# Kernel optimization log

Measured on AMD Instinct MI355X. Metric: run time of the kernel, lower is better.

## Reference

```python
import jax, jax.numpy as jnp
import numpy as np

CONTEXT = 2048
D_MODEL = 1024
HEAD = 64


def setup_inputs() -> dict:
    key = jax.random.key(0)
    kx, kk, kq, kv = jax.random.split(key, 4)
    s = 1.0 / np.sqrt(D_MODEL)  # ~ torch Linear init scale
    return {
        "x": jax.random.normal(kx, (8, CONTEXT, D_MODEL), dtype=jnp.float32),
        "Wk": jax.random.uniform(kk, (D_MODEL, HEAD), dtype=jnp.float32, minval=-s, maxval=s),
        "Wq": jax.random.uniform(kq, (D_MODEL, HEAD), dtype=jnp.float32, minval=-s, maxval=s),
        "Wv": jax.random.uniform(kv, (D_MODEL, HEAD), dtype=jnp.float32, minval=-s, maxval=s),
    }


def reference(x, Wk, Wq, Wv):
    b, t, c = x.shape
    k = jnp.einsum("btc,ch->bth", x, Wk)
    q = jnp.einsum("btc,ch->bth", x, Wq)
    v = jnp.einsum("btc,ch->bth", x, Wv)
    # NOTE: original scales by c**-0.5 (embedding dim), not head_size**-0.5
    scores = jnp.einsum("bqh,bkh->bqk", q, k) * (c ** -0.5)
    causal = jnp.tril(jnp.ones((t, t), dtype=bool))
    scores = jnp.where(causal, scores, jnp.float32(-jnp.inf))
    weights = jax.nn.softmax(scores, axis=-1)
    return jnp.einsum("bqk,bkh->bqh", weights, v)
```

## Files before the change

kernel.cpp:

```cpp
#include <hip/hip_runtime.h>
#include <hip/hip_bf16.h>

#define CTX 2048
#define DM  1024
#define HD  64
#define BATCH 8
#define NSLOT 144

typedef __attribute__((ext_vector_type(8))) short bf16x8;
typedef __attribute__((ext_vector_type(4))) float f32x4;

__device__ inline unsigned short f2bf(float f) {
    unsigned int u = __float_as_uint(f);
    unsigned int r = (u + 0x7fffu + ((u >> 16) & 1u)) >> 16;
    return (unsigned short)r;
}

__device__ inline bf16x8 pack8(const float4& f0, const float4& f1) {
    union { bf16x8 v; __hip_bfloat162 h[4]; } u;
    u.h[0] = __float22bfloat162_rn(make_float2(f0.x, f0.y));
    u.h[1] = __float22bfloat162_rn(make_float2(f0.z, f0.w));
    u.h[2] = __float22bfloat162_rn(make_float2(f1.x, f1.y));
    u.h[3] = __float22bfloat162_rn(make_float2(f1.z, f1.w));
    return u.v;
}

__device__ __forceinline__ void gload16(const void* gsrc, void* ldst) {
    __builtin_amdgcn_global_load_lds(
        (const __attribute__((address_space(1))) void*)gsrc,
        (__attribute__((address_space(3))) void*)ldst,
        16, 0, 0);
}

__device__ __forceinline__ int chunk_prefix(int qi) {
    int q4 = qi >> 2, r = qi & 3;
    return qi + 2 * q4 * (q4 - 1) + q4 * r;
}

__global__ __launch_bounds__(256) void wtrans(
    const float* __restrict__ Wq, const float* __restrict__ Wk,
    const float* __restrict__ Wv, unsigned short* __restrict__ wt)
{
    __shared__ __align__(16) unsigned short tile[64][72];
    const int m  = blockIdx.y;
    const int k0 = blockIdx.x * 64;
    const float* W = (m == 0) ? Wq : (m == 1) ? Wk : Wv;
    const int tid = threadIdx.x;
    const int c   = tid & 63, kk = tid >> 6;
    #pragma unroll
    for (int i = 0; i < 16; i++) {
        int kl = kk + i * 4;
        tile[c][kl] = f2bf(W[(size_t)(k0 + kl) * HD + c]);
    }
    __syncthreads();
    const int c2 = tid >> 2, seg = tid & 3;
    bf16x8 a = *reinterpret_cast<const bf16x8*>(&tile[c2][seg * 16]);
    bf16x8 b = *reinterpret_cast<const bf16x8*>(&tile[c2][seg * 16 + 8]);
    unsigned short* dst = wt + (size_t)(m * 64 + c2) * DM + k0 + seg * 16;
    *reinterpret_cast<bf16x8*>(dst)     = a;
    *reinterpret_cast<bf16x8*>(dst + 8) = b;
}

__global__ __launch_bounds__(512) void qkv_gemm(
    const float* __restrict__ x, const unsigned short* __restrict__ wt,
    unsigned short* __restrict__ q, unsigned short* __restrict__ k,
    unsigned short* __restrict__ vt)
{
    __shared__ __align__(16) unsigned short wsT[2][192 * 64];
    __shared__ __align__(16) unsigned short xsB[2][32 * 64];

    const int tid  = threadIdx.x, lane = tid & 63, w = tid >> 6;
    const int wr   = w >> 2, wc = w & 3;
    const int m0   = (int)blockIdx.x * 32;
    const int lcol = lane & 15, g = lane >> 4;

    const int xrow = tid >> 3;
    const int xpar = tid & 7;

    f32x4 acc[3];
    #pragma unroll
    for (int cf = 0; cf < 3; cf++) acc[cf] = (f32x4)0.f;

    float4 rxA0, rxA1, rxB0, rxB1;

    auto gloadW = [&](int k0, int buf) {
        #pragma unroll
        for (int i = 0; i < 3; i++) {
            const int cid = (w * 3 + i) * 64 + lane;
            const int c   = cid >> 3;
            const int p   = (cid & 7) ^ (c & 7);
            gload16(wt + (size_t)c * DM + k0 + p * 8,
                    &wsT[buf][(w * 3 + i) * 512]);
        }
    };
    auto ldXA = [&](int k0) {
        if (tid < 256) {
            const float* src = x + (size_t)(m0 + xrow) * DM + k0 + xpar * 8;
            rxA0 = *reinterpret_cast<const float4*>(src);
            rxA1 = *reinterpret_cast<const float4*>(src + 4);
        }
    };
    auto ldXB = [&](int k0) {
        if (tid < 256) {
            const float* src = x + (size_t)(m0 + xrow) * DM + k0 + xpar * 8;
            rxB0 = *reinterpret_cast<const float4*>(src);
            rxB1 = *reinterpret_cast<const float4*>(src + 4);
        }
    };
    auto stXA = [&](int buf) {
        if (tid < 256)
            *reinterpret_cast<bf16x8*>(reinterpret_cast<char*>(xsB[buf]) +
                ((xrow * 128 + xpar * 16) ^ ((xrow & 7) << 4))) = pack8(rxA0, rxA1);
    };
    auto stXB = [&](int buf) {
        if (tid < 256)
            *reinterpret_cast<bf16x8*>(reinterpret_cast<char*>(xsB[buf]) +
                ((xrow * 128 + xpar * 16) ^ ((xrow & 7) << 4))) = pack8(rxB0, rxB1);
    };
    auto compute = [&](int buf) {
        char* wb = reinterpret_cast<char*>(wsT[buf]);
        char* xb = reinterpret_cast<char*>(xsB[buf]);
        #pragma unroll
        for (int kc = 0; kc < 2; kc++) {
            const int arow = wr * 16 + lcol;
            bf16x8 a = *reinterpret_cast<const bf16x8*>(
                xb + ((arow * 128 + kc * 64 + g * 16) ^ ((arow & 7) << 4)));
            #pragma unroll
            for (int cf = 0; cf < 3; cf++) {
                const int c = wc * 48 + cf * 16 + lcol;
                bf16x8 b = *reinterpret_cast<const bf16x8*>(
                    wb + ((c * 128 + kc * 64 + g * 16) ^ ((c & 7) << 4)));
                acc[cf] = __builtin_amdgcn_mfma_f32_16x16x32_bf16(a, b, acc[cf], 0, 0, 0);
            }
        }
    };

    ldXA(0); ldXB(64);
    gloadW(0, 0);
    stXA(0);
    __syncthreads();

    #pragma unroll 1
    for (int t = 0; t < 16; t += 2) {
        gloadW((t + 1) * 64, 1);
        if (t + 2 < 16) ldXA((t + 2) * 64);
        compute(0);
        stXB(1);
        __syncthreads();
        if (t + 2 < 16) gloadW((t + 2) * 64, 0);
        if (t + 3 < 16) ldXB((t + 3) * 64);
        compute(1);
        if (t + 2 < 16) stXA(0);
        __syncthreads();
    }

    const float QSCALE = 0.03125f * 1.4426950408889634f;
    #pragma unroll
    for (int cf = 0; cf < 3; cf++)
        #pragma unroll
        for (int r = 0; r < 4; r++) {
            int row = m0 + wr * 16 + g * 4 + r;
            int col = wc * 48 + cf * 16 + lcol;
            int bb = row >> 11, tt = row & (CTX - 1);
            if (col < 64)       q[(size_t)row * HD + col] = f2bf(acc[cf][r] * QSCALE);
            else if (col < 128) k[(size_t)row * HD + (col - 64)] = f2bf(acc[cf][r]);
            else                vt[(size_t)bb * HD * CTX + (size_t)(col - 128) * CTX + tt] = f2bf(acc[cf][r]);
        }
}

__global__ __launch_bounds__(256) void attn_fa(
    const unsigned short* __restrict__ qg, const unsigned short* __restrict__ kg,
    const unsigned short* __restrict__ vtg, unsigned short* __restrict__ po,
    float* __restrict__ ml)
{
    __shared__ __align__(16) unsigned short ks[64 * 64];
    __shared__ __align__(16) unsigned short vs[64 * 64];
    __shared__ __align__(16) float pf[4][16 * 64];

    const int tid  = threadIdx.x, lane = tid & 63, w = tid >> 6;
    const int bid  = blockIdx.x;
    const int b    = blockIdx.y;
    int qi = 31;
    while (chunk_prefix(qi) > bid) qi--;
    const int c  = bid - chunk_prefix(qi);
    const int t0 = c * 4, t1 = min(t0 + 3, qi);
    const int rb = qi * 64 + w * 16;
    const int lcol = lane & 15, g = lane >> 4, lrow = g << 2;
    const size_t base  = (size_t)b * CTX * HD;
    const size_t vbase = (size_t)b * HD * CTX;
    char* ksb = reinterpret_cast<char*>(ks);
    char* vsb = reinterpret_cast<char*>(vs);
    char* pb  = reinterpret_cast<char*>(pf[w]);

    bf16x8 qa[2];
    #pragma unroll
    for (int kc = 0; kc < 2; kc++)
        qa[kc] = *reinterpret_cast<const bf16x8*>(
            qg + base + (size_t)(rb + lcol) * HD + kc * 32 + 8 * g);

    f32x4 o[4];
    #pragma unroll
    for (int dc = 0; dc < 4; dc++) o[dc] = (f32x4)0.f;
    float lsum[4] = {0.f, 0.f, 0.f, 0.f};

    const int r0 = tid >> 3, p0 = tid & 7, r1 = 32 + r0;
    bf16x8 kreg0, kreg1, vreg0, vreg1;

    auto ld = [&](int t) {
        const int j0 = t * 64;
        kreg0 = *reinterpret_cast<const bf16x8*>(kg + base + (size_t)(j0 + r0) * HD + p0 * 8);
        kreg1 = *reinterpret_cast<const bf16x8*>(kg + base + (size_t)(j0 + r1) * HD + p0 * 8);
        vreg0 = *reinterpret_cast<const bf16x8*>(vtg + vbase + (size_t)r0 * CTX + j0 + p0 * 8);
        vreg1 = *reinterpret_cast<const bf16x8*>(vtg + vbase + (size_t)r1 * CTX + j0 + p0 * 8);
    };
    auto st = [&]() {
        *reinterpret_cast<bf16x8*>(ksb + ((r0 * 128 + p0 * 16) ^ ((r0 & 7) << 4))) = kreg0;
        *reinterpret_cast<bf16x8*>(ksb + ((r1 * 128 + p0 * 16) ^ ((r1 & 7) << 4))) = kreg1;
        *reinterpret_cast<bf16x8*>(vsb + ((r0 * 128 + p0 * 16) ^ ((r0 & 7) << 4))) = vreg0;
        *reinterpret_cast<bf16x8*>(vsb + ((r1 * 128 + p0 * 16) ^ ((r1 & 7) << 4))) = vreg1;
    };

    ld(t0);
    for (int t = t0; t <= t1; t++) {
        __syncthreads();
        st();
        __syncthreads();
        if (t < t1) ld(t + 1);
        const int j0 = t * 64;

        f32x4 s[4];
        #pragma unroll
        for (int ch = 0; ch < 4; ch++) {
            s[ch] = (f32x4)0.f;
            #pragma unroll
            for (int kc = 0; kc < 2; kc++) {
                const int krow = ch * 16 + lcol;
                bf16x8 kf = *reinterpret_cast<const bf16x8*>(
                    ksb + ((krow * 128 + kc * 64 + g * 16) ^ ((krow & 7) << 4)));
                s[ch] = __builtin_amdgcn_mfma_f32_16x16x32_bf16(qa[kc], kf, s[ch], 0, 0, 0);
            }
        }

        if (t == qi) {
            #pragma unroll
            for (int ch = 0; ch < 4; ch++)
                #pragma unroll
                for (int r = 0; r < 4; r++)
                    if (j0 + ch * 16 + lcol > rb + lrow + r) s[ch][r] = -1e30f;
        }

        #pragma unroll
        for (int ch = 0; ch < 4; ch++)
            #pragma unroll
            for (int r = 0; r < 4; r++) {
                float p = exp2f(s[ch][r]);
                lsum[r] += p;
                const int row = lrow + r;
                *reinterpret_cast<float*>(
                    pb + ((row * 256 + (ch * 16 + lcol) * 4) ^ ((row & 7) << 4))) = p;
            }

        bf16x8 pa[2];
        const int rswz = (lcol & 7) << 4;
        #pragma unroll
        for (int kc = 0; kc < 2; kc++) {
            float4 f0 = *reinterpret_cast<const float4*>(
                pb + ((lcol * 256 + kc * 128 + g * 32) ^ rswz));
            float4 f1 = *reinterpret_cast<const float4*>(
                pb + ((lcol * 256 + kc * 128 + g * 32 + 16) ^ rswz));
            pa[kc] = pack8(f0, f1);
        }

        #pragma unroll
        for (int dc = 0; dc < 4; dc++)
            #pragma unroll
            for (int kc = 0; kc < 2; kc++) {
                const int vrow = dc * 16 + lcol;
                bf16x8 vf = *reinterpret_cast<const bf16x8*>(
                    vsb + ((vrow * 128 + kc * 64 + g * 16) ^ ((vrow & 7) << 4)));
                o[dc] = __builtin_amdgcn_mfma_f32_16x16x32_bf16(pa[kc], vf, o[dc], 0, 0, 0);
            }
    }

    const size_t sl = (size_t)b * NSLOT + bid;
    #pragma unroll
    for (int dc = 0; dc < 4; dc++)
        #pragma unroll
        for (int r = 0; r < 4; r++) {
            const int row = lrow + r;
            *reinterpret_cast<float*>(
                pb + ((row * 256 + (dc * 16 + lcol) * 4) ^ ((row & 7) << 4))) = o[dc][r];
        }
    {
        const int orow = lcol;
        const int rswz = (orow & 7) << 4;
        float4 a0 = *reinterpret_cast<const float4*>(pb + ((orow * 256 + g * 64)      ^ rswz));
        float4 a1 = *reinterpret_cast<const float4*>(pb + ((orow * 256 + g * 64 + 16) ^ rswz));
        float4 a2 = *reinterpret_cast<const float4*>(pb + ((orow * 256 + g * 64 + 32) ^ rswz));
        float4 a3 = *reinterpret_cast<const float4*>(pb + ((orow * 256 + g * 64 + 48) ^ rswz));
        unsigned short* dst = po + sl * 4096 + (size_t)(w * 16 + orow) * 64 + g * 16;
        *reinterpret_cast<bf16x8*>(dst)     = pack8(a0, a1);
        *reinterpret_cast<bf16x8*>(dst + 8) = pack8(a2, a3);
    }
    #pragma unroll
    for (int r = 0; r < 4; r++) {
        float x = lsum[r];
        x += __shfl_xor(x, 1);
        x += __shfl_xor(x, 2);
        x += __shfl_xor(x, 4);
        x += __shfl_xor(x, 8);
        lsum[r] = x;
    }
    if (lcol == 0) {
        #pragma unroll
        for (int r = 0; r < 4; r++)
            ml[sl * 64 + w * 16 + lrow + r] = lsum[r];
    }
}

__global__ __launch_bounds__(256) void attn_merge(
    const unsigned short* __restrict__ po, const float* __restrict__ ml,
    float* __restrict__ out)
{
    const int qi = blockIdx.x, b = blockIdx.y;
    const int nch = (qi >> 2) + 1;
    const int s0  = chunk_prefix(qi);
    const int f8  = threadIdx.x & 7;
    const int r0  = threadIdx.x >> 3;
    const size_t obase = (size_t)b * CTX * HD;

    #pragma unroll
    for (int half = 0; half < 2; half++) {
        const int row = half * 32 + r0;
        float L = 0.f;
        float acc[8];
        #pragma unroll
        for (int j = 0; j < 8; j++) acc[j] = 0.f;
        for (int cc = 0; cc < nch; cc++) {
            size_t sl = (size_t)b * NSLOT + s0 + cc;
            L += ml[sl * 64 + row];
            bf16x8 v8 = *reinterpret_cast<const bf16x8*>(po + sl * 4096 + (size_t)row * 64 + f8 * 8);
            #pragma unroll
            for (int j = 0; j < 8; j++)
                acc[j] += __uint_as_float(((unsigned)(unsigned short)v8[j]) << 16);
        }
        const float inv = 1.f / L;
        float4 o0 = make_float4(acc[0] * inv, acc[1] * inv, acc[2] * inv, acc[3] * inv);
        float4 o1 = make_float4(acc[4] * inv, acc[5] * inv, acc[6] * inv, acc[7] * inv);
        float* dst = out + obase + (size_t)(qi * 64 + row) * HD + f8 * 8;
        *reinterpret_cast<float4*>(dst)     = o0;
        *reinterpret_cast<float4*>(dst + 4) = o1;
    }
}

extern "C" void kernel_launch(void* const* d_in, const int* in_sizes, int n_in,
                              void* d_out, int out_size, void* d_ws, size_t ws_size,
                              hipStream_t stream) {
    const float* x  = (const float*)d_in[0];
    const float* Wk = (const float*)d_in[1];
    const float* Wq = (const float*)d_in[2];
    const float* Wv = (const float*)d_in[3];
    float* outp = (float*)d_out;

    const size_t n = (size_t)BATCH * CTX * HD;
    unsigned short* qb  = (unsigned short*)d_ws;
    unsigned short* kb  = qb + n;
    unsigned short* vtb = kb + n;
    unsigned short* wtb = vtb + n;
    unsigned short* pob = wtb + 192 * 1024;
    float*          mlb = (float*)(pob + (size_t)BATCH * NSLOT * 4096);

    wtrans<<<dim3(16, 3), dim3(256), 0, stream>>>(Wq, Wk, Wv, wtb);
    qkv_gemm<<<dim3(16384 / 32), dim3(512), 0, stream>>>(x, wtb, qb, kb, vtb);
    attn_fa<<<dim3(NSLOT, BATCH), dim3(256), 0, stream>>>(qb, kb, vtb, pob, mlb);
    attn_merge<<<dim3(32, BATCH), dim3(256), 0, stream>>>(pob, mlb, outp);
}
```

Measured before the change: 53.15 us.

## Deepen x-prefetch pipeline in QKV projection with manual waitcnt and sched barriers

Restructures the QKV projection main loop to keep four register stages of x loads in flight instead of two. It replaces __syncthreads with explicit s_waitcnt vmcnt/lgkmcnt plus s_barrier and sched_barrier fences, so global loads can overlap compute across several iterations. Out-of-range tile indices are clamped rather than branched, which issues a few redundant loads at the tail. The cost is more live registers and fragile hand-counted vmcnt values that must match the number of outstanding loads.

```diff
diff --git a/kernel.cpp b/kernel.cpp
--- a/kernel.cpp
+++ b/kernel.cpp
@@ -81,7 +81,7 @@
     #pragma unroll
     for (int cf = 0; cf < 3; cf++) acc[cf] = (f32x4)0.f;
 
-    float4 rxA0, rxA1, rxB0, rxB1;
+    float4 rx00, rx01, rx10, rx11, rx20, rx21, rx30, rx31;
 
     auto gloadW = [&](int k0, int buf) {
         #pragma unroll
@@ -93,30 +93,6 @@
                     &wsT[buf][(w * 3 + i) * 512]);
         }
     };
-    auto ldXA = [&](int k0) {
-        if (tid < 256) {
-            const float* src = x + (size_t)(m0 + xrow) * DM + k0 + xpar * 8;
-            rxA0 = *reinterpret_cast<const float4*>(src);
-            rxA1 = *reinterpret_cast<const float4*>(src + 4);
-        }
-    };
-    auto ldXB = [&](int k0) {
-        if (tid < 256) {
-            const float* src = x + (size_t)(m0 + xrow) * DM + k0 + xpar * 8;
-            rxB0 = *reinterpret_cast<const float4*>(src);
-            rxB1 = *reinterpret_cast<const float4*>(src + 4);
-        }
-    };
-    auto stXA = [&](int buf) {
-        if (tid < 256)
-            *reinterpret_cast<bf16x8*>(reinterpret_cast<char*>(xsB[buf]) +
-                ((xrow * 128 + xpar * 16) ^ ((xrow & 7) << 4))) = pack8(rxA0, rxA1);
-    };
-    auto stXB = [&](int buf) {
-        if (tid < 256)
-            *reinterpret_cast<bf16x8*>(reinterpret_cast<char*>(xsB[buf]) +
-                ((xrow * 128 + xpar * 16) ^ ((xrow & 7) << 4))) = pack8(rxB0, rxB1);
-    };
     auto compute = [&](int buf) {
         char* wb = reinterpret_cast<char*>(wsT[buf]);
         char* xb = reinterpret_cast<char*>(xsB[buf]);
@@ -135,24 +111,52 @@
         }
     };
 
-    ldXA(0); ldXB(64);
+#define LDX(S, T) do { if (tid < 256) { \
+        int _t = (T); _t = _t > 15 ? 15 : _t; \
+        const float* _s = x + (size_t)(m0 + xrow) * DM + _t * 64 + xpar * 8; \
+        rx##S##0 = *reinterpret_cast<const float4*>(_s); \
+        rx##S##1 = *reinterpret_cast<const float4*>(_s + 4); } } while (0)
+
+#define STX(S, BUF) do { if (tid < 256) \
+        *reinterpret_cast<bf16x8*>(reinterpret_cast<char*>(xsB[BUF]) + \
+            ((xrow * 128 + xpar * 16) ^ ((xrow & 7) << 4))) = pack8(rx##S##0, rx##S##1); \
+    } while (0)
+
+#define PHASE(K, SST, SLD, BUF) do { \
+        STX(SST, (BUF) ^ 1); \
+        __builtin_amdgcn_sched_barrier(0); \
+        LDX(SLD, t + (K) + 4); \
+        __builtin_amdgcn_sched_barrier(0); \
+        compute(BUF); \
+        asm volatile("s_waitcnt vmcnt(2) lgkmcnt(0)" ::: "memory"); \
+        __builtin_amdgcn_s_barrier(); \
+        __builtin_amdgcn_sched_barrier(0); \
+        { int _wk = t + (K) + 2; _wk = _wk > 15 ? 15 : _wk; gloadW(_wk * 64, BUF); } \
+        __builtin_amdgcn_sched_barrier(0); \
+    } while (0)
+
     gloadW(0, 0);
-    stXA(0);
-    __syncthreads();
+    __builtin_amdgcn_sched_barrier(0);
+    LDX(0, 0); LDX(1, 1); LDX(2, 2); LDX(3, 3);
+    __builtin_amdgcn_sched_barrier(0);
+    STX(0, 0);
+    __builtin_amdgcn_sched_barrier(0);
+    asm volatile("s_waitcnt vmcnt(6) lgkmcnt(0)" ::: "memory");
+    __builtin_amdgcn_s_barrier();
+    __builtin_amdgcn_sched_barrier(0);
+    gloadW(64, 1);
+    __builtin_amdgcn_sched_barrier(0);
 
     #pragma unroll 1
-    for (int t = 0; t < 16; t += 2) {
-        gloadW((t + 1) * 64, 1);
-        if (t + 2 < 16) ldXA((t + 2) * 64);
-        compute(0);
-        stXB(1);
-        __syncthreads();
-        if (t + 2 < 16) gloadW((t + 2) * 64, 0);
-        if (t + 3 < 16) ldXB((t + 3) * 64);
-        compute(1);
-        if (t + 2 < 16) stXA(0);
-        __syncthreads();
-    }
+    for (int t = 0; t < 16; t += 4) {
+        PHASE(0, 1, 0, 0);
+        PHASE(1, 2, 1, 1);
+        PHASE(2, 3, 2, 0);
+        PHASE(3, 0, 3, 1);
+    }
+#undef PHASE
+#undef STX
+#undef LDX
 
     const float QSCALE = 0.03125f * 1.4426950408889634f;
     #pragma unroll
```

Result: slower. 56.87 us (+7.0%).

## Load QKV weight fragments directly into registers instead of staging through LDS

Applied to the files above, without the earlier changes.

The QKV projection kernel no longer stages the transposed bf16 weights in double-buffered shared memory via global_load_lds. Each lane now loads its own B-operand fragments from global memory into two register sets and feeds them straight to the MFMAs, with the loads for the next tile issued after the current tile's compute. This removes the LDS traffic and shared-memory footprint for weights. In exchange it raises register pressure and duplicates global weight reads across the two warp rows (served from cache).

```diff
diff --git a/kernel.cpp b/kernel.cpp
--- a/kernel.cpp
+++ b/kernel.cpp
@@ -23,13 +23,6 @@
     u.h[2] = __float22bfloat162_rn(make_float2(f1.x, f1.y));
     u.h[3] = __float22bfloat162_rn(make_float2(f1.z, f1.w));
     return u.v;
-}
-
-__device__ __forceinline__ void gload16(const void* gsrc, void* ldst) {
-    __builtin_amdgcn_global_load_lds(
-        (const __attribute__((address_space(1))) void*)gsrc,
-        (__attribute__((address_space(3))) void*)ldst,
-        16, 0, 0);
 }
 
 __device__ __forceinline__ int chunk_prefix(int qi) {
@@ -66,7 +59,6 @@
     unsigned short* __restrict__ q, unsigned short* __restrict__ k,
     unsigned short* __restrict__ vt)
 {
-    __shared__ __align__(16) unsigned short wsT[2][192 * 64];
     __shared__ __align__(16) unsigned short xsB[2][32 * 64];
 
     const int tid  = threadIdx.x, lane = tid & 63, w = tid >> 6;
@@ -77,21 +69,30 @@
     const int xrow = tid >> 3;
     const int xpar = tid & 7;
 
+    const unsigned short* wp = wt + (size_t)(wc * 48 + lcol) * DM + g * 8;
+
     f32x4 acc[3];
     #pragma unroll
     for (int cf = 0; cf < 3; cf++) acc[cf] = (f32x4)0.f;
 
+    bf16x8 rwA[6], rwB[6];
     float4 rxA0, rxA1, rxB0, rxB1;
 
-    auto gloadW = [&](int k0, int buf) {
-        #pragma unroll
-        for (int i = 0; i < 3; i++) {
-            const int cid = (w * 3 + i) * 64 + lane;
-            const int c   = cid >> 3;
-            const int p   = (cid & 7) ^ (c & 7);
-            gload16(wt + (size_t)c * DM + k0 + p * 8,
-                    &wsT[buf][(w * 3 + i) * 512]);
-        }
+    auto ldWA = [&](int k0) {
+        #pragma unroll
+        for (int cf = 0; cf < 3; cf++)
+            #pragma unroll
+            for (int kc = 0; kc < 2; kc++)
+                rwA[cf * 2 + kc] = *reinterpret_cast<const bf16x8*>(
+                    wp + (size_t)cf * 16 * DM + k0 + kc * 32);
+    };
+    auto ldWB = [&](int k0) {
+        #pragma unroll
+        for (int cf = 0; cf < 3; cf++)
+            #pragma unroll
+            for (int kc = 0; kc < 2; kc++)
+                rwB[cf * 2 + kc] = *reinterpret_cast<const bf16x8*>(
+                    wp + (size_t)cf * 16 * DM + k0 + kc * 32);
     };
     auto ldXA = [&](int k0) {
         if (tid < 256) {
@@ -117,39 +118,46 @@
             *reinterpret_cast<bf16x8*>(reinterpret_cast<char*>(xsB[buf]) +
                 ((xrow * 128 + xpar * 16) ^ ((xrow & 7) << 4))) = pack8(rxB0, rxB1);
     };
-    auto compute = [&](int buf) {
-        char* wb = reinterpret_cast<char*>(wsT[buf]);
-        char* xb = reinterpret_cast<char*>(xsB[buf]);
+    auto computeA = [&]() {
+        char* xb = reinterpret_cast<char*>(xsB[0]);
+        const int arow = wr * 16 + lcol;
         #pragma unroll
         for (int kc = 0; kc < 2; kc++) {
-            const int arow = wr * 16 + lcol;
             bf16x8 a = *reinterpret_cast<const bf16x8*>(
                 xb + ((arow * 128 + kc * 64 + g * 16) ^ ((arow & 7) << 4)));
             #pragma unroll
-            for (int cf = 0; cf < 3; cf++) {
-                const int c = wc * 48 + cf * 16 + lcol;
-                bf16x8 b = *reinterpret_cast<const bf16x8*>(
-                    wb + ((c * 128 + kc * 64 + g * 16) ^ ((c & 7) << 4)));
-                acc[cf] = __builtin_amdgcn_mfma_f32_16x16x32_bf16(a, b, acc[cf], 0, 0, 0);
-            }
-        }
-    };
-
+            for (int cf = 0; cf < 3; cf++)
+                acc[cf] = __builtin_amdgcn_mfma_f32_16x16x32_bf16(a, rwA[cf * 2 + kc], acc[cf], 0, 0, 0);
+        }
+    };
+    auto computeB = [&]() {
+        char* xb = reinterpret_cast<char*>(xsB[1]);
+        const int arow = wr * 16 + lcol;
+        #pragma unroll
+        for (int kc = 0; kc < 2; kc++) {
+            bf16x8 a = *reinterpret_cast<const bf16x8*>(
+                xb + ((arow * 128 + kc * 64 + g * 16) ^ ((arow & 7) << 4)));
+            #pragma unroll
+            for (int cf = 0; cf < 3; cf++)
+                acc[cf] = __builtin_amdgcn_mfma_f32_16x16x32_bf16(a, rwB[cf * 2 + kc], acc[cf], 0, 0, 0);
+        }
+    };
+
+    ldWA(0); ldWB(64);
     ldXA(0); ldXB(64);
-    gloadW(0, 0);
     stXA(0);
     __syncthreads();
 
     #pragma unroll 1
     for (int t = 0; t < 16; t += 2) {
-        gloadW((t + 1) * 64, 1);
         if (t + 2 < 16) ldXA((t + 2) * 64);
-        compute(0);
+        computeA();
+        if (t + 2 < 16) ldWA((t + 2) * 64);
         stXB(1);
         __syncthreads();
-        if (t + 2 < 16) gloadW((t + 2) * 64, 0);
         if (t + 3 < 16) ldXB((t + 3) * 64);
-        compute(1);
+        computeB();
+        if (t + 3 < 16) ldWB((t + 3) * 64);
         if (t + 2 < 16) stXA(0);
         __syncthreads();
     }
```

After: 83.19 us. 1.57x slower.
